# Kernel optimization log

Hardware: AMD Instinct MI355X
Metric: run time of the kernel (lower is better)

The kernel has to match this reference:

```python
import jax, jax.numpy as jnp
import numpy as np

EMBED_DIM = 1024
NUM_HEADS = 16
HEAD_DIM = EMBED_DIM // NUM_HEADS
SCALE = HEAD_DIM ** -0.5


def setup_inputs() -> dict:
    key = jax.random.key(0)
    ks = jax.random.split(key, 12)
    B, S, D = 4, 2048, EMBED_DIM
    x = jax.random.normal(ks[0], (B, S, D), dtype=jnp.float32)
    key_padding_mask = jax.random.randint(ks[1], (B, S), 0, 2).astype(jnp.bool_)
    init = 1.0 / np.sqrt(D)
    def lin(kw, kb):
        W = jax.random.uniform(kw, (D, D), minval=-init, maxval=init, dtype=jnp.float32)
        b = jax.random.uniform(kb, (D,), minval=-init, maxval=init, dtype=jnp.float32)
        return W, b
    Wq, bq = lin(ks[2], ks[3])
    Wk, bk = lin(ks[4], ks[5])
    Wv, bv = lin(ks[6], ks[7])
    Wo, bo = lin(ks[8], ks[9])
    return {"x": x, "key_padding_mask": key_padding_mask,
            "Wq": Wq, "bq": bq, "Wk": Wk, "bk": bk,
            "Wv": Wv, "bv": bv, "Wo": Wo, "bo": bo}


def reference(x, key_padding_mask, Wq, bq, Wk, bk, Wv, bv, Wo, bo):
    B, S, D = x.shape
    H, Hd = NUM_HEADS, HEAD_DIM
    # projections (torch Linear: y = x @ W.T + b)
    q = (x @ Wq.T + bq).reshape(B, S, H, Hd).transpose(0, 2, 1, 3)  # [B,H,S,Hd]
    k = (x @ Wk.T + bk).reshape(B, S, H, Hd).transpose(0, 2, 1, 3)
    v = (x @ Wv.T + bv).reshape(B, S, H, Hd).transpose(0, 2, 1, 3)
    scores = jnp.einsum('bhqd,bhkd->bhqk', q, k) * SCALE  # [B,H,S,S]
    mask = key_padding_mask[:, None, None, :]  # [B,1,1,S]
    scores = jnp.where(mask, -jnp.inf, scores)
    probs = jax.nn.softmax(scores, axis=-1)
    # dropout p=0.0 (inference) -> identity
    out = jnp.einsum('bhqk,bhkd->bhqd', probs, v)  # [B,H,S,Hd]
    out = out.transpose(0, 2, 1, 3).reshape(B, S, D)
    return out @ Wo.T + bo
```

## Files before the change

### kernel.cpp

```cpp
#include <hip/hip_runtime.h>
#include <stdint.h>

typedef __bf16 bf16;
typedef __bf16 bf16x8 __attribute__((ext_vector_type(8)));
typedef float f32x4 __attribute__((ext_vector_type(4)));

#define SEQ 2048
#define NHEAD 16
#define HDIM 64
#define DMODEL 1024
#define NBATCH 4
#define ATT_SCALE 0.18033688011112042f
#define SEQHD (SEQ * HDIM)
#define BHSTRIDE (2 * SEQHD)


__device__ __forceinline__ void gload_lds16(const bf16* g, bf16* l) {
  __builtin_amdgcn_global_load_lds(
      (const __attribute__((address_space(1))) uint32_t*)g,
      (__attribute__((address_space(3))) uint32_t*)l, 16, 0, 0);
}

__device__ __forceinline__ uint32_t pk2(float a, float b) {
  bf16 x = (bf16)a, y = (bf16)b;
  return (uint32_t)__builtin_bit_cast(uint16_t, x) |
         ((uint32_t)__builtin_bit_cast(uint16_t, y) << 16);
}

__global__ __launch_bounds__(256) void cvt_kernel(const float* __restrict__ src,
                                                  bf16* __restrict__ dst) {
  size_t i = ((size_t)blockIdx.x * 256 + threadIdx.x) * 16;
#pragma unroll
  for (int j = 0; j < 2; ++j) {
    float4 f0 = *(const float4*)(src + i + j * 8);
    float4 f1 = *(const float4*)(src + i + j * 8 + 4);
    bf16x8 v;
    v[0] = (bf16)f0.x; v[1] = (bf16)f0.y; v[2] = (bf16)f0.z; v[3] = (bf16)f0.w;
    v[4] = (bf16)f1.x; v[5] = (bf16)f1.y; v[6] = (bf16)f1.z; v[7] = (bf16)f1.w;
    *(bf16x8*)(dst + i + j * 8) = v;
  }
}

__global__ __launch_bounds__(256) void cvt3_kernel(const float* __restrict__ a,
                                                   const float* __restrict__ b,
                                                   const float* __restrict__ c,
                                                   bf16* __restrict__ dst) {
  const float* s = blockIdx.y == 0 ? a : (blockIdx.y == 1 ? b : c);
  bf16* d = dst + (size_t)blockIdx.y * DMODEL * DMODEL;
  size_t i = ((size_t)blockIdx.x * 256 + threadIdx.x) * 16;
#pragma unroll
  for (int j = 0; j < 2; ++j) {
    float4 f0 = *(const float4*)(s + i + j * 8);
    float4 f1 = *(const float4*)(s + i + j * 8 + 4);
    bf16x8 v;
    v[0] = (bf16)f0.x; v[1] = (bf16)f0.y; v[2] = (bf16)f0.z; v[3] = (bf16)f0.w;
    v[4] = (bf16)f1.x; v[5] = (bf16)f1.y; v[6] = (bf16)f1.z; v[7] = (bf16)f1.w;
    *(bf16x8*)(d + i + j * 8) = v;
  }
}

__global__ __launch_bounds__(256) void scan_kernel(int* __restrict__ posv) {
  __shared__ int sums[256];
  const int b = blockIdx.x, t = threadIdx.x;
  int* m = posv + b * SEQ;
  int f[8], cnt = 0;
#pragma unroll
  for (int j = 0; j < 8; ++j) {
    int x = m[t * 8 + j];
    int unm = (x < 0) ? 0 : ((x & 0x40000000) ? 1 : (x == 0 ? 1 : 0));
    f[j] = unm; cnt += unm;
  }
  sums[t] = cnt;
  __syncthreads();
  if (t == 0) {
    int acc = 0;
#pragma unroll 8
    for (int i = 0; i < 256; ++i) { int s = sums[i]; sums[i] = acc; acc += s; }
  }
  __syncthreads();
  int p = sums[t];
#pragma unroll
  for (int j = 0; j < 8; ++j) {
    m[t * 8 + j] = (int)((f[j] ? 0x40000000u : 0x80000000u) | (unsigned)p);
    p += f[j];
  }
}

__global__ __launch_bounds__(256) void proj_kernel(
    const bf16* __restrict__ xb, const bf16* __restrict__ Wall,
    const float* __restrict__ bq, const float* __restrict__ bk,
    const float* __restrict__ bv, const int* __restrict__ posv,
    bf16* __restrict__ Qall, bf16* __restrict__ kv, int b_base) {
  __shared__ __align__(16) bf16 lW[64 * 64];
  __shared__ __align__(16) bf16 lXw[4][64 * 64];
  const int t = threadIdx.x, wave = t >> 6, lane = t & 63;
  const int quad = lane >> 4, c = lane & 15;
  const int m0 = blockIdx.x * 256;
  const int nt = blockIdx.y;
  const int sel = nt >> 4, h = nt & 15;
  const bf16* W = Wall + (size_t)sel * DMODEL * DMODEL + (size_t)(h * HDIM) * DMODEL;
  bf16* pw = lXw[wave];
  const int sr = lane >> 3, sg = lane & 7;
  const bf16* aS = xb + (size_t)(m0 + wave * 64 + sr) * DMODEL + ((sg ^ sr) * 8);
  const bf16* wS = W + (size_t)(wave * 8 + sr) * DMODEL + ((sg ^ sr) * 8);
  f32x4 acc[4][4] = {};
  for (int k0 = 0; k0 < DMODEL; k0 += 64) {
    __syncthreads();
    gload_lds16(wS + k0, lW + wave * 512);
    gload_lds16(wS + 32 * DMODEL + k0, lW + wave * 512 + 2048);
#pragma unroll
    for (int ii = 0; ii < 8; ++ii)
      gload_lds16(aS + k0 + (size_t)ii * 8 * DMODEL, pw + ii * 512);
    __syncthreads();
#pragma unroll
    for (int kk = 0; kk < 2; ++kk) {
      bf16x8 af[4], bfr[4];
#pragma unroll
      for (int mi = 0; mi < 4; ++mi) {
        int row = mi * 16 + c;
        af[mi] = *(const bf16x8*)(pw + row * 64 + (((kk * 4 + quad) ^ (row & 7)) * 8));
      }
#pragma unroll
      for (int ni = 0; ni < 4; ++ni) {
        int row = ni * 16 + c;
        bfr[ni] = *(const bf16x8*)(lW + row * 64 + (((kk * 4 + quad) ^ (row & 7)) * 8));
      }
#pragma unroll
      for (int mi = 0; mi < 4; ++mi)
#pragma unroll
        for (int ni = 0; ni < 4; ++ni)
          acc[mi][ni] = __builtin_amdgcn_mfma_f32_16x16x32_bf16(af[mi], bfr[ni], acc[mi][ni], 0, 0, 0);
    }
  }

  if (sel == 0) {
#pragma unroll
    for (int ni = 0; ni < 4; ++ni) {
      int hd = ni * 16 + c;
      float bqv = bq[h * HDIM + hd];
#pragma unroll
      for (int mi = 0; mi < 4; ++mi)
#pragma unroll
        for (int r = 0; r < 4; ++r) {
          int tok = m0 + wave * 64 + mi * 16 + quad * 4 + r;
          int b_loc = tok >> 11, s = tok & 2047;
          Qall[((size_t)((b_base + b_loc) * NHEAD + h) * SEQ + s) * HDIM + hd] =
              (bf16)((acc[mi][ni][r] + bqv) * ATT_SCALE);
        }
    }
  } else {
    const float* bias = (sel == 1 ? bk : bv) + h * HDIM;
    const int isV = (sel == 2);
    const int b_loc0 = m0 >> 11;
    int v2 = posv[b_loc0 * SEQ + SEQ - 1];
    int nk = (v2 & 0x3FFFFFFF) + (v2 >= 0 ? 1 : 0);
    bf16* base = kv + (size_t)(b_loc0 * NHEAD + h) * BHSTRIDE;
#pragma unroll
    for (int ni = 0; ni < 4; ++ni) {
      int hd = ni * 16 + c;
      float bv_ = bias[hd];
#pragma unroll
      for (int mi = 0; mi < 4; ++mi)
#pragma unroll
        for (int r = 0; r < 4; ++r) {
          int tok = m0 + wave * 64 + mi * 16 + quad * 4 + r;
          int s = tok & 2047;
          int pv = posv[b_loc0 * SEQ + s];
          int pos = pv & 0x3FFFFFFF;
          int dst = (pv >= 0) ? pos : (nk + (s - pos));
          float val = (pv >= 0) ? (acc[mi][ni][r] + bv_) : 0.0f;
          if (isV) base[SEQHD + (size_t)hd * SEQ + dst] = (bf16)val;
          else     base[(size_t)dst * HDIM + hd] = (bf16)val;
        }
    }
  }
}

__global__ __launch_bounds__(256, 4) void attn4_kernel(
    const bf16* __restrict__ Qall, const bf16* __restrict__ KV,
    const int* __restrict__ posv, bf16* __restrict__ O, int chunk) {
  __shared__ __align__(16) bf16 lK[64 * 64];
  __shared__ __align__(16) bf16 lV[64 * 64];
  __shared__ __align__(16) bf16 lPw[4][16 * 64];
  const int t = threadIdx.x, wave = t >> 6, lane = t & 63;
  const int quad = lane >> 4, c = lane & 15;
  const int i = blockIdx.x;
  const int xcd = i & 7, slot = i >> 3;
  const int bhl = xcd * 4 + (slot >> 5);
  const int qt = slot & 31;
  const int b_loc = bhl >> 4, h = bhl & 15;
  const int b = chunk * 2 + b_loc;
  const int q0 = qt * 64 + wave * 16;
  const bf16* Qh = Qall + (size_t)(b * NHEAD + h) * SEQHD;
  const bf16* Kb = KV + (size_t)(b_loc * NHEAD + h) * BHSTRIDE;
  const bf16* Vtb = Kb + SEQHD;
  bf16* pw = lPw[wave];

  int v2 = posv[b * SEQ + SEQ - 1];
  int nk = (v2 & 0x3FFFFFFF) + (v2 >= 0 ? 1 : 0);
  int NT = ((nk + 63) >> 6) << 6;

  const int srow = t >> 3;
  const int sswz = (t & 7) ^ (srow & 7);
  const bf16* kSrc = Kb + (size_t)srow * HDIM + sswz * 8;
  const bf16* vSrc = Vtb + (size_t)srow * SEQ + sswz * 8;
  bf16* kDst = lK + wave * 512;
  bf16* vDst = lV + wave * 512;

  bf16x8 qf[2];
#pragma unroll
  for (int kk = 0; kk < 2; ++kk)
    qf[kk] = *(const bf16x8*)(Qh + (size_t)(q0 + c) * HDIM + kk * 32 + quad * 8);

  f32x4 oacc[4] = {};
  float mrun = -1e30f, lrun = 0.0f;

  const int pbase = c * 64 + (quad & 1) * 4;
  const int pswz = c & 7;

#pragma unroll
  for (int i2 = 0; i2 < 2; ++i2) {
    gload_lds16(kSrc + i2 * 32 * HDIM, kDst + i2 * 2048);
    gload_lds16(vSrc + (size_t)i2 * 32 * SEQ, vDst + i2 * 2048);
  }
  __syncthreads();

  for (int kt = 0; kt < NT; kt += 64) {
    f32x4 sacc[4] = {};
#pragma unroll
    for (int kk = 0; kk < 2; ++kk) {
      bf16x8 kf[4];
#pragma unroll
      for (int ni = 0; ni < 4; ++ni) {
        int row = ni * 16 + c;
        kf[ni] = *(const bf16x8*)(lK + row * 64 + (((kk * 4 + quad) ^ (row & 7)) * 8));
      }
#pragma unroll
      for (int ni = 0; ni < 4; ++ni)
        sacc[ni] = __builtin_amdgcn_mfma_f32_16x16x32_bf16(kf[ni], qf[kk], sacc[ni], 0, 0, 0);
    }

    __syncthreads();
    if (kt + 64 < NT) {
      const bf16* ks = kSrc + (size_t)(kt + 64) * HDIM;
#pragma unroll
      for (int i2 = 0; i2 < 2; ++i2) gload_lds16(ks + i2 * 32 * HDIM, kDst + i2 * 2048);
    }

    if (kt + 64 > nk) {
      int base = kt + quad * 4 - nk;
#pragma unroll
      for (int ni = 0; ni < 4; ++ni)
#pragma unroll
        for (int r = 0; r < 4; ++r)
          if (base + ni * 16 + r >= 0) sacc[ni][r] = -3e38f;
    }

    float mx = sacc[0][0];
#pragma unroll
    for (int ni = 0; ni < 4; ++ni)
#pragma unroll
      for (int r = 0; r < 4; ++r)
        if (ni | r) mx = fmaxf(mx, sacc[ni][r]);
    mx = fmaxf(mx, __shfl_xor(mx, 16));
    mx = fmaxf(mx, __shfl_xor(mx, 32));
    float mn = fmaxf(mrun, mx);
    float al = __builtin_amdgcn_exp2f(mrun - mn);
    mrun = mn;
    float rs = 0.0f;
#pragma unroll
    for (int ni = 0; ni < 4; ++ni)
#pragma unroll
      for (int r = 0; r < 4; ++r) {
        float e = __builtin_amdgcn_exp2f(sacc[ni][r] - mn);
        sacc[ni][r] = e; rs += e;
      }
    rs += __shfl_xor(rs, 16);
    rs += __shfl_xor(rs, 32);
    lrun = lrun * al + rs;

#pragma unroll
    for (int ni = 0; ni < 4; ++ni) {
      uint32_t u0 = pk2(sacc[ni][0], sacc[ni][1]);
      uint32_t u1 = pk2(sacc[ni][2], sacc[ni][3]);
      int sl = pbase + (((ni * 2 + (quad >> 1)) ^ pswz) * 8);
      *(uint32_t*)(pw + sl) = u0;
      *(uint32_t*)(pw + sl + 2) = u1;
    }

    float al4[4];
#pragma unroll
    for (int r = 0; r < 4; ++r) al4[r] = __shfl(al, quad * 4 + r);
#pragma unroll
    for (int ni = 0; ni < 4; ++ni)
#pragma unroll
      for (int r = 0; r < 4; ++r) oacc[ni][r] *= al4[r];

#pragma unroll
    for (int kk = 0; kk < 2; ++kk) {
      bf16x8 pf, vfr[4];
      pf = *(const bf16x8*)(pw + c * 64 + (((kk * 4 + quad) ^ (c & 7)) * 8));
#pragma unroll
      for (int ni = 0; ni < 4; ++ni) {
        int row = ni * 16 + c;
        vfr[ni] = *(const bf16x8*)(lV + row * 64 + (((kk * 4 + quad) ^ (row & 7)) * 8));
      }
#pragma unroll
      for (int ni = 0; ni < 4; ++ni)
        oacc[ni] = __builtin_amdgcn_mfma_f32_16x16x32_bf16(pf, vfr[ni], oacc[ni], 0, 0, 0);
    }

    __syncthreads();
    if (kt + 64 < NT) {
      const bf16* vs = vSrc + (kt + 64);
#pragma unroll
      for (int i2 = 0; i2 < 2; ++i2) gload_lds16(vs + (size_t)i2 * 32 * SEQ, vDst + i2 * 2048);
    }
  }

  float linv = lrun > 0.0f ? 1.0f / lrun : 0.0f;
  float linv4[4];
#pragma unroll
  for (int r = 0; r < 4; ++r) linv4[r] = __shfl(linv, quad * 4 + r);
#pragma unroll
  for (int r = 0; r < 4; ++r) {
    size_t tok = (size_t)b * SEQ + q0 + quad * 4 + r;
#pragma unroll
    for (int ni = 0; ni < 4; ++ni)
      O[tok * DMODEL + h * HDIM + ni * 16 + c] = (bf16)(oacc[ni][r] * linv4[r]);
  }
}

__global__ __launch_bounds__(256) void outproj_kernel(
    const bf16* __restrict__ O, const bf16* __restrict__ Wob,
    const float* __restrict__ bo, float* __restrict__ out) {
  __shared__ __align__(16) bf16 lW[64 * 64];
  __shared__ __align__(16) bf16 lXw[4][64 * 64];
  const int t = threadIdx.x, wave = t >> 6, lane = t & 63;
  const int quad = lane >> 4, c = lane & 15;
  const int m0 = blockIdx.x * 256;
  const int n0 = blockIdx.y * 64;
  bf16* pw = lXw[wave];
  const int sr = lane >> 3, sg = lane & 7;
  const bf16* aS = O + (size_t)(m0 + wave * 64 + sr) * DMODEL + ((sg ^ sr) * 8);
  const bf16* wS = Wob + (size_t)(n0 + wave * 8 + sr) * DMODEL + ((sg ^ sr) * 8);
  f32x4 acc[4][4] = {};
  for (int k0 = 0; k0 < DMODEL; k0 += 64) {
    __syncthreads();
    gload_lds16(wS + k0, lW + wave * 512);
    gload_lds16(wS + 32 * DMODEL + k0, lW + wave * 512 + 2048);
#pragma unroll
    for (int ii = 0; ii < 8; ++ii)
      gload_lds16(aS + k0 + (size_t)ii * 8 * DMODEL, pw + ii * 512);
    __syncthreads();
#pragma unroll
    for (int kk = 0; kk < 2; ++kk) {
      bf16x8 af[4], bfr[4];
#pragma unroll
      for (int mi = 0; mi < 4; ++mi) {
        int row = mi * 16 + c;
        af[mi] = *(const bf16x8*)(pw + row * 64 + (((kk * 4 + quad) ^ (row & 7)) * 8));
      }
#pragma unroll
      for (int ni = 0; ni < 4; ++ni) {
        int row = ni * 16 + c;
        bfr[ni] = *(const bf16x8*)(lW + row * 64 + (((kk * 4 + quad) ^ (row & 7)) * 8));
      }
#pragma unroll
      for (int mi = 0; mi < 4; ++mi)
#pragma unroll
        for (int ni = 0; ni < 4; ++ni)
          acc[mi][ni] = __builtin_amdgcn_mfma_f32_16x16x32_bf16(af[mi], bfr[ni], acc[mi][ni], 0, 0, 0);
    }
  }
#pragma unroll
  for (int ni = 0; ni < 4; ++ni) {
    int gn = n0 + ni * 16 + c;
    float bv_ = bo[gn];
#pragma unroll
    for (int mi = 0; mi < 4; ++mi)
#pragma unroll
      for (int r = 0; r < 4; ++r) {
        int gm = m0 + wave * 64 + mi * 16 + quad * 4 + r;
        out[(size_t)gm * DMODEL + gn] = acc[mi][ni][r] + bv_;
      }
  }
}

extern "C" void kernel_launch(void* const* d_in, const int* in_sizes, int n_in,
                              void* d_out, int out_size, void* d_ws, size_t ws_size,
                              hipStream_t stream) {
  const float* x  = (const float*)d_in[0];
  int*         posv = (int*)d_in[1];
  const float* Wq = (const float*)d_in[2]; const float* bq = (const float*)d_in[3];
  const float* Wk = (const float*)d_in[4]; const float* bk = (const float*)d_in[5];
  const float* Wv = (const float*)d_in[6]; const float* bv = (const float*)d_in[7];
  const float* Wo = (const float*)d_in[8]; const float* bo = (const float*)d_in[9];
  float* out = (float*)d_out;
  char* outc = (char*)d_out;
  char* xc   = (char*)d_in[0];
  const size_t half = (size_t)NBATCH * SEQ * DMODEL * 2;
  const size_t qtr  = half / 2;

  bf16* Qall = (bf16*)d_out;
  bf16* xbf  = (bf16*)(outc + half);
  bf16* KV   = (bf16*)xc;
  bf16* O    = (bf16*)(xc + half);
  bf16* Wbf3 = (bf16*)(xc + half + qtr);
  bf16* Wobf = (bf16*)xc;

  scan_kernel<<<dim3(NBATCH), 256, 0, stream>>>(posv);
  cvt_kernel<<<dim3(2048), 256, 0, stream>>>(x, xbf);
  cvt3_kernel<<<dim3(256, 3), 256, 0, stream>>>(Wq, Wk, Wv, Wbf3);
  proj_kernel<<<dim3(16, 48), 256, 0, stream>>>(xbf, Wbf3, bq, bk, bv, posv, Qall, KV, 0);
  attn4_kernel<<<dim3(1024), 256, 0, stream>>>(Qall, KV, posv, O, 0);
  proj_kernel<<<dim3(16, 48), 256, 0, stream>>>(xbf + (size_t)2 * SEQ * DMODEL, Wbf3, bq, bk, bv,
                                                posv + 2 * SEQ, Qall, KV, 2);
  attn4_kernel<<<dim3(1024), 256, 0, stream>>>(Qall, KV, posv, O, 1);
  cvt_kernel<<<dim3(256), 256, 0, stream>>>(Wo, Wobf);
  outproj_kernel<<<dim3(32, 16), 256, 0, stream>>>(O, Wobf, bo, out);
}
```

Baseline: 324.4 us.

## Split Q and KV projections and compute K/V only for unmasked tokens

The scan kernel now also builds an inverse index of unmasked token positions. The fused projection is split into a Q projection over all tokens, run once for the whole batch, and a K/V projection that gathers only unmasked rows of x. K/V blocks past the unmasked count exit early, and a small kernel zero-fills the padding up to the next 64-row tile. This removes the masked-key share of the K/V GEMM work (about half with the random mask). The cost is gathered row loads, two extra kernel launches and an extra index buffer placed in reused input memory.

```diff
diff --git a/kernel.cpp b/kernel.cpp
--- a/kernel.cpp
+++ b/kernel.cpp
@@ -59,16 +59,19 @@
   }
 }
 
-__global__ __launch_bounds__(256) void scan_kernel(int* __restrict__ posv) {
+__global__ __launch_bounds__(256) void scan_kernel(int* __restrict__ posv,
+                                                   int* __restrict__ inv) {
   __shared__ int sums[256];
   const int b = blockIdx.x, t = threadIdx.x;
   int* m = posv + b * SEQ;
+  int* iv = inv + b * SEQ;
   int f[8], cnt = 0;
 #pragma unroll
   for (int j = 0; j < 8; ++j) {
     int x = m[t * 8 + j];
     int unm = (x < 0) ? 0 : ((x & 0x40000000) ? 1 : (x == 0 ? 1 : 0));
     f[j] = unm; cnt += unm;
+    iv[t * 8 + j] = 0;
   }
   sums[t] = cnt;
   __syncthreads();
@@ -82,23 +85,21 @@
 #pragma unroll
   for (int j = 0; j < 8; ++j) {
     m[t * 8 + j] = (int)((f[j] ? 0x40000000u : 0x80000000u) | (unsigned)p);
+    if (f[j]) iv[p] = t * 8 + j;
     p += f[j];
   }
 }
 
-__global__ __launch_bounds__(256) void proj_kernel(
+__global__ __launch_bounds__(256) void qproj_kernel(
     const bf16* __restrict__ xb, const bf16* __restrict__ Wall,
-    const float* __restrict__ bq, const float* __restrict__ bk,
-    const float* __restrict__ bv, const int* __restrict__ posv,
-    bf16* __restrict__ Qall, bf16* __restrict__ kv, int b_base) {
+    const float* __restrict__ bq, bf16* __restrict__ Qall) {
   __shared__ __align__(16) bf16 lW[64 * 64];
   __shared__ __align__(16) bf16 lXw[4][64 * 64];
   const int t = threadIdx.x, wave = t >> 6, lane = t & 63;
   const int quad = lane >> 4, c = lane & 15;
   const int m0 = blockIdx.x * 256;
-  const int nt = blockIdx.y;
-  const int sel = nt >> 4, h = nt & 15;
-  const bf16* W = Wall + (size_t)sel * DMODEL * DMODEL + (size_t)(h * HDIM) * DMODEL;
+  const int h = blockIdx.y;
+  const bf16* W = Wall + (size_t)(h * HDIM) * DMODEL;
   bf16* pw = lXw[wave];
   const int sr = lane >> 3, sg = lane & 7;
   const bf16* aS = xb + (size_t)(m0 + wave * 64 + sr) * DMODEL + ((sg ^ sr) * 8);
@@ -132,47 +133,111 @@
           acc[mi][ni] = __builtin_amdgcn_mfma_f32_16x16x32_bf16(af[mi], bfr[ni], acc[mi][ni], 0, 0, 0);
     }
   }
-
-  if (sel == 0) {
-#pragma unroll
-    for (int ni = 0; ni < 4; ++ni) {
-      int hd = ni * 16 + c;
-      float bqv = bq[h * HDIM + hd];
+#pragma unroll
+  for (int ni = 0; ni < 4; ++ni) {
+    int hd = ni * 16 + c;
+    float bqv = bq[h * HDIM + hd];
+#pragma unroll
+    for (int mi = 0; mi < 4; ++mi)
+#pragma unroll
+      for (int r = 0; r < 4; ++r) {
+        int tok = m0 + wave * 64 + mi * 16 + quad * 4 + r;
+        int b = tok >> 11, s = tok & 2047;
+        Qall[((size_t)(b * NHEAD + h) * SEQ + s) * HDIM + hd] =
+            (bf16)((acc[mi][ni][r] + bqv) * ATT_SCALE);
+      }
+  }
+}
+
+__global__ __launch_bounds__(256) void kvproj_kernel(
+    const bf16* __restrict__ xb, const bf16* __restrict__ Wall,
+    const float* __restrict__ bk, const float* __restrict__ bv,
+    const int* __restrict__ posv, const int* __restrict__ inv,
+    bf16* __restrict__ kv) {
+  __shared__ __align__(16) bf16 lW[64 * 64];
+  __shared__ __align__(16) bf16 lXw[4][64 * 64];
+  const int t = threadIdx.x, wave = t >> 6, lane = t & 63;
+  const int quad = lane >> 4, c = lane & 15;
+  const int bx = blockIdx.x;
+  const int b_loc = bx >> 3, mb = bx & 7;
+  const int nt = blockIdx.y;
+  const int isV = nt >> 4, h = nt & 15;
+  int v2 = posv[b_loc * SEQ + SEQ - 1];
+  int nk = (v2 & 0x3FFFFFFF) + (v2 >= 0 ? 1 : 0);
+  const int c0 = mb * 256;
+  if (c0 >= nk) return;
+  const bf16* W = Wall + (size_t)(1 + isV) * DMODEL * DMODEL + (size_t)(h * HDIM) * DMODEL;
+  const float* bias = (isV ? bv : bk) + h * HDIM;
+  bf16* pw = lXw[wave];
+  const int sr = lane >> 3, sg = lane & 7;
+  const int swzc = (sg ^ sr) * 8;
+  const bf16* wS = W + (size_t)(wave * 8 + sr) * DMODEL + swzc;
+  const int* invb = inv + b_loc * SEQ;
+  int grow[8];
+#pragma unroll
+  for (int ii = 0; ii < 8; ++ii)
+    grow[ii] = invb[c0 + wave * 64 + ii * 8 + sr];
+  const bf16* xbb = xb + (size_t)b_loc * SEQ * DMODEL + swzc;
+  f32x4 acc[4][4] = {};
+  for (int k0 = 0; k0 < DMODEL; k0 += 64) {
+    __syncthreads();
+    gload_lds16(wS + k0, lW + wave * 512);
+    gload_lds16(wS + 32 * DMODEL + k0, lW + wave * 512 + 2048);
+#pragma unroll
+    for (int ii = 0; ii < 8; ++ii)
+      gload_lds16(xbb + (size_t)grow[ii] * DMODEL + k0, pw + ii * 512);
+    __syncthreads();
+#pragma unroll
+    for (int kk = 0; kk < 2; ++kk) {
+      bf16x8 af[4], bfr[4];
+#pragma unroll
+      for (int mi = 0; mi < 4; ++mi) {
+        int row = mi * 16 + c;
+        af[mi] = *(const bf16x8*)(pw + row * 64 + (((kk * 4 + quad) ^ (row & 7)) * 8));
+      }
+#pragma unroll
+      for (int ni = 0; ni < 4; ++ni) {
+        int row = ni * 16 + c;
+        bfr[ni] = *(const bf16x8*)(lW + row * 64 + (((kk * 4 + quad) ^ (row & 7)) * 8));
+      }
 #pragma unroll
       for (int mi = 0; mi < 4; ++mi)
 #pragma unroll
-        for (int r = 0; r < 4; ++r) {
-          int tok = m0 + wave * 64 + mi * 16 + quad * 4 + r;
-          int b_loc = tok >> 11, s = tok & 2047;
-          Qall[((size_t)((b_base + b_loc) * NHEAD + h) * SEQ + s) * HDIM + hd] =
-              (bf16)((acc[mi][ni][r] + bqv) * ATT_SCALE);
-        }
-    }
-  } else {
-    const float* bias = (sel == 1 ? bk : bv) + h * HDIM;
-    const int isV = (sel == 2);
-    const int b_loc0 = m0 >> 11;
-    int v2 = posv[b_loc0 * SEQ + SEQ - 1];
-    int nk = (v2 & 0x3FFFFFFF) + (v2 >= 0 ? 1 : 0);
-    bf16* base = kv + (size_t)(b_loc0 * NHEAD + h) * BHSTRIDE;
-#pragma unroll
-    for (int ni = 0; ni < 4; ++ni) {
-      int hd = ni * 16 + c;
-      float bv_ = bias[hd];
-#pragma unroll
-      for (int mi = 0; mi < 4; ++mi)
-#pragma unroll
-        for (int r = 0; r < 4; ++r) {
-          int tok = m0 + wave * 64 + mi * 16 + quad * 4 + r;
-          int s = tok & 2047;
-          int pv = posv[b_loc0 * SEQ + s];
-          int pos = pv & 0x3FFFFFFF;
-          int dst = (pv >= 0) ? pos : (nk + (s - pos));
-          float val = (pv >= 0) ? (acc[mi][ni][r] + bv_) : 0.0f;
-          if (isV) base[SEQHD + (size_t)hd * SEQ + dst] = (bf16)val;
-          else     base[(size_t)dst * HDIM + hd] = (bf16)val;
-        }
-    }
+        for (int ni = 0; ni < 4; ++ni)
+          acc[mi][ni] = __builtin_amdgcn_mfma_f32_16x16x32_bf16(af[mi], bfr[ni], acc[mi][ni], 0, 0, 0);
+    }
+  }
+  bf16* base = kv + (size_t)(b_loc * NHEAD + h) * BHSTRIDE;
+#pragma unroll
+  for (int ni = 0; ni < 4; ++ni) {
+    int hd = ni * 16 + c;
+    float bv_ = bias[hd];
+#pragma unroll
+    for (int mi = 0; mi < 4; ++mi)
+#pragma unroll
+      for (int r = 0; r < 4; ++r) {
+        int dst = c0 + wave * 64 + mi * 16 + quad * 4 + r;
+        float val = acc[mi][ni][r] + bv_;
+        if (isV) base[SEQHD + (size_t)hd * SEQ + dst] = (bf16)val;
+        else     base[(size_t)dst * HDIM + hd] = (bf16)val;
+      }
+  }
+}
+
+__global__ __launch_bounds__(256) void zf_kernel(bf16* __restrict__ kv,
+                                                 const int* __restrict__ posv) {
+  const int bh = blockIdx.x, t = threadIdx.x;
+  const int b_loc = bh >> 4, h = bh & 15;
+  int v2 = posv[b_loc * SEQ + SEQ - 1];
+  int nk = (v2 & 0x3FFFFFFF) + (v2 >= 0 ? 1 : 0);
+  int NT = ((nk + 63) >> 6) << 6;
+  int pad = NT - nk;
+  if (pad == 0) return;
+  bf16* base = kv + (size_t)(b_loc * NHEAD + h) * BHSTRIDE;
+  int hd = t & 63;
+  for (int rr = t >> 6; rr < pad; rr += 4) {
+    base[(size_t)(nk + rr) * HDIM + hd] = (bf16)0.0f;
+    base[SEQHD + (size_t)hd * SEQ + nk + rr] = (bf16)0.0f;
   }
 }
 
@@ -407,15 +472,19 @@
   bf16* KV   = (bf16*)xc;
   bf16* O    = (bf16*)(xc + half);
   bf16* Wbf3 = (bf16*)(xc + half + qtr);
+  int*  inv  = (int*)(xc + half + qtr + (size_t)3 * DMODEL * DMODEL * 2);
   bf16* Wobf = (bf16*)xc;
 
-  scan_kernel<<<dim3(NBATCH), 256, 0, stream>>>(posv);
   cvt_kernel<<<dim3(2048), 256, 0, stream>>>(x, xbf);
+  scan_kernel<<<dim3(NBATCH), 256, 0, stream>>>(posv, inv);
   cvt3_kernel<<<dim3(256, 3), 256, 0, stream>>>(Wq, Wk, Wv, Wbf3);
-  proj_kernel<<<dim3(16, 48), 256, 0, stream>>>(xbf, Wbf3, bq, bk, bv, posv, Qall, KV, 0);
+  qproj_kernel<<<dim3(32, 16), 256, 0, stream>>>(xbf, Wbf3, bq, Qall);
+  kvproj_kernel<<<dim3(16, 32), 256, 0, stream>>>(xbf, Wbf3, bk, bv, posv, inv, KV);
+  zf_kernel<<<dim3(32), 256, 0, stream>>>(KV, posv);
   attn4_kernel<<<dim3(1024), 256, 0, stream>>>(Qall, KV, posv, O, 0);
-  proj_kernel<<<dim3(16, 48), 256, 0, stream>>>(xbf + (size_t)2 * SEQ * DMODEL, Wbf3, bq, bk, bv,
-                                                posv + 2 * SEQ, Qall, KV, 2);
+  kvproj_kernel<<<dim3(16, 32), 256, 0, stream>>>(xbf + (size_t)2 * SEQ * DMODEL, Wbf3, bk, bv,
+                                                  posv + 2 * SEQ, inv + 2 * SEQ, KV);
+  zf_kernel<<<dim3(32), 256, 0, stream>>>(KV, posv + 2 * SEQ);
   attn4_kernel<<<dim3(1024), 256, 0, stream>>>(Qall, KV, posv, O, 1);
   cvt_kernel<<<dim3(256), 256, 0, stream>>>(Wo, Wobf);
   outproj_kernel<<<dim3(32, 16), 256, 0, stream>>>(O, Wobf, bo, out);
```

Result: faster. 311.7 us (-3.9%).
